# Performance work log

Measured on AMD Instinct MI355X. Metric: run time of the kernel, lower is better.

Reference implementation:

```python
import jax, jax.numpy as jnp
import numpy as np

# (a1,a2,a3,a4,b1,b2,b3,b4,xi_E,xi_I,mu,e,k) per oscillator type
PARAMS = {
    1: (0.0, 5.0, 5.0, 1.0, 0.0, -1.0, 1.0, 0.0, 0.0, 0.0, 5.0, 0.001, 500),
    2: (0.5, 0.55, 0.55, -0.5, 0.5, -0.55, -0.55, -0.5, 0.0, 0.0, 1.0, 0.001, 50),
    3: (0.5, 0.6, 0.55, 0.5, -0.5, -0.6, -0.55, 0.5, 0.0, 0.0, 1.0, 0.001, 50),
    4: (-0.5, 0.55, 0.55, -0.5, -0.5, -0.55, -0.55, 0.5, 0.0, 0.0, 1.0, 0.001, 50),
    5: (-0.9, 0.9, 0.9, -0.9, 0.9, -0.9, -0.9, 0.9, 0.0, 0.0, 1.0, 0.001, 50),
    6: (-0.9, 0.9, 0.9, -0.9, 0.9, -0.9, -0.9, 0.9, 0.0, 0.0, 1.0, 0.001, 300),
    7: (-5.0, 5.0, 5.0, -5.0, 1.0, -1.0, -1.0, 1.0, 0.0, 0.0, 1.0, 0.001, 50),
    8: (-5.0, 5.0, 5.0, -5.0, 1.0, -1.0, -1.0, 1.0, 0.0, 0.0, 1.0, 0.001, 300),
}
N_STEPS = 100  # torch runs t = 0..99 producing LORS[1..100], then max over those


def _lee_forward(x, osc_type):
    a1, a2, a3, a4, b1, b2, b3, b4, xi_E, xi_I, mu, e, k = PARAMS[osc_type]
    # stimulus with tiny sign-dependent offset; constant over time
    sim0 = x + e * jnp.sign(x)
    damp = jnp.exp(-k * sim0 * sim0)   # exp(-k*sim0^2), constant over time
    omega = jnp.tanh(mu * sim0)        # Omega[t+1] is the same every step
    E0 = jnp.full_like(x, 0.2)
    I0 = jnp.zeros_like(x)
    L0 = jnp.full_like(x, 0.2)
    m0 = jnp.full_like(x, -jnp.inf)    # running max over LORS[1..100]

    def step(carry, _):
        E, I, L, m = carry
        E1 = jnp.tanh(mu * (a1 * L + a2 * E - a3 * I + a4 * sim0 - xi_E))
        I1 = jnp.tanh(mu * (b1 * L - b2 * E - b3 * I + b4 * sim0 - xi_I))
        L1 = (E1 - I1) * damp + omega
        return (E1, I1, L1, jnp.maximum(m, L1)), None

    (_, _, _, m), _ = jax.lax.scan(step, (E0, I0, L0, m0), None, length=N_STEPS)
    return m


def setup_inputs() -> dict:
    key = jax.random.key(0)
    x = jax.random.normal(key, (2048, 512), dtype=jnp.float32)
    return {"x": x, "oscillator_type": 1}


def reference(x, oscillator_type):
    # output shape == x.shape: time-max-pooled LORS activation
    return _lee_forward(x, oscillator_type)
```

## Files before the change

### kernel.cpp

```cpp
#include <hip/hip_runtime.h>
#include <math.h>


#define N_STEPS 100

typedef float v2f __attribute__((ext_vector_type(2)));
__device__ __forceinline__ v2f splat2(float s){ v2f v; v.x = s; v.y = s; return v; }

__constant__ float PAR[8][13] = {
    { 0.0f,  5.0f,  5.0f,  1.0f,  0.0f, -1.0f,  1.0f,  0.0f, 0.0f, 0.0f, 5.0f, 0.001f, 500.0f},
    { 0.5f,  0.55f, 0.55f, -0.5f,  0.5f, -0.55f, -0.55f, -0.5f, 0.0f, 0.0f, 1.0f, 0.001f, 50.0f},
    { 0.5f,  0.6f,  0.55f,  0.5f, -0.5f, -0.6f,  -0.55f,  0.5f, 0.0f, 0.0f, 1.0f, 0.001f, 50.0f},
    {-0.5f,  0.55f, 0.55f, -0.5f, -0.5f, -0.55f, -0.55f,  0.5f, 0.0f, 0.0f, 1.0f, 0.001f, 50.0f},
    {-0.9f,  0.9f,  0.9f,  -0.9f,  0.9f, -0.9f,  -0.9f,   0.9f, 0.0f, 0.0f, 1.0f, 0.001f, 50.0f},
    {-0.9f,  0.9f,  0.9f,  -0.9f,  0.9f, -0.9f,  -0.9f,   0.9f, 0.0f, 0.0f, 1.0f, 0.001f, 300.0f},
    {-5.0f,  5.0f,  5.0f,  -5.0f,  1.0f, -1.0f,  -1.0f,   1.0f, 0.0f, 0.0f, 1.0f, 0.001f, 50.0f},
    {-5.0f,  5.0f,  5.0f,  -5.0f,  1.0f, -1.0f,  -1.0f,   1.0f, 0.0f, 0.0f, 1.0f, 0.001f, 300.0f},
};

__device__ __forceinline__ float xla_tanhf(float x) {
#pragma clang fp contract(off)
    float ax = fabsf(x);
    float xc = fminf(fmaxf(x, -7.99881172180175781f), 7.99881172180175781f);
    float x2 = xc * xc;
    float p = -2.76076847742355e-16f;
    p = fmaf(p, x2, 2.00018790482477e-13f);
    p = fmaf(p, x2, -8.60467152213735e-11f);
    p = fmaf(p, x2, 5.12229709037114e-08f);
    p = fmaf(p, x2, 1.48572235717979e-05f);
    p = fmaf(p, x2, 6.37261928875436e-04f);
    p = fmaf(p, x2, 4.89352455891786e-03f);
    float num = xc * p;
    float q = 1.19825839466702e-06f;
    q = fmaf(q, x2, 1.18534705686654e-04f);
    q = fmaf(q, x2, 2.26843463243900e-03f);
    q = fmaf(q, x2, 4.89352518554385e-03f);
    float r = num / q;
    return (ax < 0.0004f) ? x : r;
}

__device__ __forceinline__ v2f div2_exact(v2f a, v2f b) {
#pragma clang fp contract(off)
    v2f r;
    r.x = __builtin_amdgcn_rcpf(b.x);
    r.y = __builtin_amdgcn_rcpf(b.y);
    v2f one = splat2(1.0f);
    v2f nb; nb.x = -b.x; nb.y = -b.y;
    v2f e  = __builtin_elementwise_fma(nb, r, one);
    r = __builtin_elementwise_fma(e, r, r);
    v2f e2 = __builtin_elementwise_fma(nb, r, one);
    r = __builtin_elementwise_fma(e2, r, r);
    v2f y = a * r;
    v2f rem = __builtin_elementwise_fma(nb, y, a);
    y = __builtin_elementwise_fma(rem, r, y);
    return y;
}

__device__ __forceinline__ v2f xla_tanh2(v2f x) {
#pragma clang fp contract(off)
    const float C = 7.99881172180175781f;
    v2f xc = __builtin_elementwise_min(__builtin_elementwise_max(x, splat2(-C)), splat2(C));
    v2f x2 = xc * xc;
    v2f p = splat2(-2.76076847742355e-16f);
    p = __builtin_elementwise_fma(p, x2, splat2(2.00018790482477e-13f));
    p = __builtin_elementwise_fma(p, x2, splat2(-8.60467152213735e-11f));
    p = __builtin_elementwise_fma(p, x2, splat2(5.12229709037114e-08f));
    p = __builtin_elementwise_fma(p, x2, splat2(1.48572235717979e-05f));
    p = __builtin_elementwise_fma(p, x2, splat2(6.37261928875436e-04f));
    p = __builtin_elementwise_fma(p, x2, splat2(4.89352455891786e-03f));
    v2f num = xc * p;
    v2f q = splat2(1.19825839466702e-06f);
    q = __builtin_elementwise_fma(q, x2, splat2(1.18534705686654e-04f));
    q = __builtin_elementwise_fma(q, x2, splat2(2.26843463243900e-03f));
    q = __builtin_elementwise_fma(q, x2, splat2(4.89352518554385e-03f));
    v2f d = div2_exact(num, q);
    v2f r;
    r.x = (fabsf(x.x) < 0.0004f) ? x.x : d.x;
    r.y = (fabsf(x.y) < 0.0004f) ? x.y : d.y;
    return r;
}

__device__ __forceinline__ float xla_expf(float x) {
#pragma clang fp contract(off)
    float xc = fminf(fmaxf(x, -88.3762626647949f), 88.3762626647950f);
    float fx = floorf(fmaf(xc, 1.44269504088896341f, 0.5f));
    float r = fmaf(fx, -0.693359375f, xc);
    r = fmaf(fx, 2.12194440e-4f, r);
    float r2 = r * r;
    float y = 1.9875691500e-4f;
    y = fmaf(y, r, 1.3981999507e-3f);
    y = fmaf(y, r, 8.3334519073e-3f);
    y = fmaf(y, r, 4.1665795894e-2f);
    y = fmaf(y, r, 1.6666665459e-1f);
    y = fmaf(y, r, 5.0000001201e-1f);
    y = fmaf(y, r2, r);
    y = y + 1.0f;
    int n2 = (int)fx;
    float p2n = __int_as_float((n2 + 127) << 23);
    return y * p2n;
}

__device__ __forceinline__ void preamble(float xv, const float* p,
                                         float& sim0, float& damp, float& omega) {
#pragma clang fp contract(off)
    float mu = p[10], e = p[11], k = p[12];
    float sgn  = (xv > 0.0f) ? 1.0f : ((xv < 0.0f) ? -1.0f : 0.0f);
    sim0 = fmaf(e, sgn, xv);
    float targ = (-k * sim0) * sim0;
    damp  = xla_expf(targ);
    omega = xla_tanhf(mu * sim0);
}

__device__ __forceinline__ bool fast_omega(float damp, float omega) {
    return (2.0f * damp) < (fabsf(omega) * 0x1p-26f);
}

__device__ __forceinline__ bool slow_t1(float xv, float e) {
#pragma clang fp contract(off)
    float sgn  = (xv > 0.0f) ? 1.0f : ((xv < 0.0f) ? -1.0f : 0.0f);
    float sim0 = fmaf(e, sgn, xv);
    return fabsf(sim0) <= 0.21f;
}

__device__ __forceinline__ float loop_t1(float sim0, float damp, float omega) {
#pragma clang fp contract(off)
    float E = 0.2f, I = 0.0f;
    float Dmax = -INFINITY;
    for (int s = 0; s < N_STEPS; ++s) {
        float tE = 5.0f * E;
        v2f mulc; mulc.x = -5.0f; mulc.y = -1.0f;
        v2f iv   = splat2(I);
        v2f addv; addv.x = tE;    addv.y = E;
        v2f u = __builtin_elementwise_fma(mulc, iv, addv);
        float sE = u.x + sim0;
        v2f pre; pre.x = sE; pre.y = u.y;
        v2f args = splat2(5.0f) * pre;
        v2f t = xla_tanh2(args);
        float D = t.x - t.y;
        Dmax = fmaxf(Dmax, D);
        E = t.x; I = t.y;
    }
    return fmaf(Dmax, damp, omega);
}

__device__ __forceinline__ float loop_gen(const float* p, float sim0,
                                          float damp, float omega) {
#pragma clang fp contract(off)
    float a1 = p[0], a2 = p[1], a3 = p[2], a4 = p[3];
    float b1 = p[4], b2 = p[5], b3 = p[6], b4 = p[7];
    float xiE = p[8], xiI = p[9], mu = p[10];
    float nb2 = -b2;
    float E = 0.2f, I = 0.0f, L = 0.2f;
    float m = -INFINITY;
    for (int s = 0; s < N_STEPS; ++s) {
        float tE = a2 * E;
        float uE = fmaf(a1, L, tE);
        uE = fmaf(-a3, I, uE);
        uE = fmaf(a4, sim0, uE);
        uE = uE - xiE;
        float argE = mu * uE;
        float tI = nb2 * E;
        float uI = fmaf(b1, L, tI);
        uI = fmaf(-b3, I, uI);
        uI = fmaf(b4, sim0, uI);
        uI = uI - xiI;
        float argI = mu * uI;
        float E1 = xla_tanhf(argE);
        float I1 = xla_tanhf(argI);
        float d = E1 - I1;
        L = fmaf(d, damp, omega);
        E = E1; I = I1;
        m = fmaxf(m, L);
    }
    return m;
}

__device__ __forceinline__ bool classify_slow(float xv, int t, const float* p) {
    if (t == 1) return slow_t1(xv, p[11]);
    float sim0, damp, omega;
    preamble(xv, p, sim0, damp, omega);
    return !fast_omega(damp, omega);
}


__global__ __launch_bounds__(256)
void k_count(const float* __restrict__ x, const int* __restrict__ osc_type,
             unsigned* __restrict__ bcount, int n)
{
    __shared__ unsigned wc[4];
    int i = blockIdx.x * 256 + threadIdx.x;
    int t = *osc_type;
    const float* p = PAR[t - 1];
    bool slow = (i < n) && classify_slow(x[i], t, p);
    unsigned long long mask = __ballot(slow);
    int lane = threadIdx.x & 63, wid = threadIdx.x >> 6;
    if (lane == 0) wc[wid] = (unsigned)__popcll(mask);
    __syncthreads();
    if (threadIdx.x == 0) bcount[blockIdx.x] = wc[0] + wc[1] + wc[2] + wc[3];
}

__global__ __launch_bounds__(256)
void k_fill(const float* __restrict__ x, const int* __restrict__ osc_type,
            float* __restrict__ out, unsigned* __restrict__ bcount,
            unsigned* __restrict__ wl, int n, int NB)
{
#pragma clang fp contract(off)
    __shared__ unsigned sums[256];
    __shared__ unsigned woff[4];
    int tid = threadIdx.x;
    int bid = blockIdx.x;

    unsigned s = 0;
    for (int j = tid; j < bid; j += 256) s += bcount[j];
    sums[tid] = s;
    __syncthreads();
    for (int off = 128; off > 0; off >>= 1) {
        if (tid < off) sums[tid] += sums[tid + off];
        __syncthreads();
    }
    unsigned bbase = sums[0];

    int i = bid * 256 + tid;
    bool active = (i < n);
    int t = *osc_type;
    const float* p = PAR[t - 1];
    float xv = active ? x[i] : 1.0e9f;
    bool slow = active && classify_slow(xv, t, p);
    if (active && !slow) {
        float mu = p[10], e = p[11];
        float sgn  = (xv > 0.0f) ? 1.0f : ((xv < 0.0f) ? -1.0f : 0.0f);
        float sim0 = fmaf(e, sgn, xv);
        out[i] = xla_tanhf(mu * sim0);
    }
    unsigned long long mask = __ballot(slow);
    int lane = tid & 63, wid = tid >> 6;
    if (lane == 0) woff[wid] = (unsigned)__popcll(mask);
    __syncthreads();
    if (slow) {
        unsigned base = bbase;
        for (int w = 0; w < wid; ++w) base += woff[w];
        base += (unsigned)__popcll(mask & ((1ull << lane) - 1ull));
        wl[base] = (unsigned)i;
    }
    if (tid == 0 && bid == NB - 1)
        bcount[NB] = bbase + woff[0] + woff[1] + woff[2] + woff[3];
}

__global__ __launch_bounds__(64)
void k_process(const float* __restrict__ x, const int* __restrict__ osc_type,
               float* __restrict__ out, const unsigned* __restrict__ total_p,
               const unsigned* __restrict__ wl)
{
#pragma clang fp contract(off)
    unsigned total = *total_p;
    int t = *osc_type;
    const float* p = PAR[t - 1];
    unsigned stride = gridDim.x * 64u;
    for (unsigned tid = blockIdx.x * 64u + threadIdx.x; tid < total; tid += stride) {
        int i = (int)wl[tid];
        float sim0, damp, omega;
        preamble(x[i], p, sim0, damp, omega);
        out[i] = (t == 1) ? loop_t1(sim0, damp, omega)
                          : loop_gen(p, sim0, damp, omega);
    }
}

__global__ __launch_bounds__(256)
void k_monolithic(const float* __restrict__ x, const int* __restrict__ osc_type,
                  float* __restrict__ out, int n)
{
#pragma clang fp contract(off)
    int i = blockIdx.x * 256 + threadIdx.x;
    if (i >= n) return;
    int t = *osc_type;
    const float* p = PAR[t - 1];
    float sim0, damp, omega;
    preamble(x[i], p, sim0, damp, omega);
    if (fast_omega(damp, omega)) { out[i] = omega; return; }
    out[i] = (t == 1) ? loop_t1(sim0, damp, omega)
                      : loop_gen(p, sim0, damp, omega);
}

extern "C" void kernel_launch(void* const* d_in, const int* in_sizes, int n_in,
                              void* d_out, int out_size, void* d_ws, size_t ws_size,
                              hipStream_t stream) {
    const float* x        = (const float*)d_in[0];
    const int*   osc_type = (const int*)d_in[1];
    float*       out      = (float*)d_out;
    int n = in_sizes[0];
    int NB = (n + 255) / 256;

    size_t needed = ((size_t)NB + 1 + (size_t)n) * sizeof(unsigned);
    if (ws_size >= needed) {
        unsigned* bcount = (unsigned*)d_ws;
        unsigned* wl     = bcount + NB + 1;
        k_count  <<<NB, 256, 0, stream>>>(x, osc_type, bcount, n);
        k_fill   <<<NB, 256, 0, stream>>>(x, osc_type, out, bcount, wl, n, NB);
        k_process<<<4096, 64, 0, stream>>>(x, osc_type, out, bcount + NB, wl);
    } else {
        k_monolithic<<<NB, 256, 0, stream>>>(x, osc_type, out, n);
    }
}
```

Before: 42.03 us.

## Fuse count, fill and process into one kernel with block-local compaction

Replaces the three-kernel pipeline (count slow elements, global prefix-scan fill of a worklist, then a separate processing grid) with a single kernel. Each block classifies its 256 elements, writes fast results directly, and compacts slow elements' index, sim0, damp and omega into shared memory. One wavefront then runs the 100-step loops over that local list. This removes two launches, the per-block O(NB) prefix summation and the global worklist traffic. The cost is that load balancing is confined to each block, and three of the four waves sit idle during the loop.

```diff
diff --git a/kernel.cpp b/kernel.cpp
--- a/kernel.cpp
+++ b/kernel.cpp
@@ -115,10 +115,7 @@
     return (2.0f * damp) < (fabsf(omega) * 0x1p-26f);
 }
 
-__device__ __forceinline__ bool slow_t1(float xv, float e) {
-#pragma clang fp contract(off)
-    float sgn  = (xv > 0.0f) ? 1.0f : ((xv < 0.0f) ? -1.0f : 0.0f);
-    float sim0 = fmaf(e, sgn, xv);
+__device__ __forceinline__ bool slow_t1_from_sim0(float sim0) {
     return fabsf(sim0) <= 0.21f;
 }
 
@@ -175,110 +172,51 @@
     return m;
 }
 
-__device__ __forceinline__ bool classify_slow(float xv, int t, const float* p) {
-    if (t == 1) return slow_t1(xv, p[11]);
-    float sim0, damp, omega;
-    preamble(xv, p, sim0, damp, omega);
-    return !fast_omega(damp, omega);
-}
-
-
 __global__ __launch_bounds__(256)
-void k_count(const float* __restrict__ x, const int* __restrict__ osc_type,
-             unsigned* __restrict__ bcount, int n)
+void k_fused(const float* __restrict__ x, const int* __restrict__ osc_type,
+             float* __restrict__ out, int n)
 {
+#pragma clang fp contract(off)
     __shared__ unsigned wc[4];
-    int i = blockIdx.x * 256 + threadIdx.x;
-    int t = *osc_type;
-    const float* p = PAR[t - 1];
-    bool slow = (i < n) && classify_slow(x[i], t, p);
-    unsigned long long mask = __ballot(slow);
-    int lane = threadIdx.x & 63, wid = threadIdx.x >> 6;
-    if (lane == 0) wc[wid] = (unsigned)__popcll(mask);
-    __syncthreads();
-    if (threadIdx.x == 0) bcount[blockIdx.x] = wc[0] + wc[1] + wc[2] + wc[3];
-}
-
-__global__ __launch_bounds__(256)
-void k_fill(const float* __restrict__ x, const int* __restrict__ osc_type,
-            float* __restrict__ out, unsigned* __restrict__ bcount,
-            unsigned* __restrict__ wl, int n, int NB)
-{
-#pragma clang fp contract(off)
-    __shared__ unsigned sums[256];
-    __shared__ unsigned woff[4];
+    __shared__ unsigned sidx[256];
+    __shared__ float    ssim[256], sdamp[256], somega[256];
+
     int tid = threadIdx.x;
-    int bid = blockIdx.x;
-
-    unsigned s = 0;
-    for (int j = tid; j < bid; j += 256) s += bcount[j];
-    sums[tid] = s;
-    __syncthreads();
-    for (int off = 128; off > 0; off >>= 1) {
-        if (tid < off) sums[tid] += sums[tid + off];
-        __syncthreads();
-    }
-    unsigned bbase = sums[0];
-
-    int i = bid * 256 + tid;
+    int i = blockIdx.x * 256 + tid;
     bool active = (i < n);
     int t = *osc_type;
     const float* p = PAR[t - 1];
+
     float xv = active ? x[i] : 1.0e9f;
-    bool slow = active && classify_slow(xv, t, p);
-    if (active && !slow) {
-        float mu = p[10], e = p[11];
-        float sgn  = (xv > 0.0f) ? 1.0f : ((xv < 0.0f) ? -1.0f : 0.0f);
-        float sim0 = fmaf(e, sgn, xv);
-        out[i] = xla_tanhf(mu * sim0);
-    }
+    float sim0, damp, omega;
+    preamble(xv, p, sim0, damp, omega);
+    bool slow;
+    if (t == 1) slow = active && slow_t1_from_sim0(sim0);
+    else        slow = active && !fast_omega(damp, omega);
+    if (active && !slow) out[i] = omega;
+
     unsigned long long mask = __ballot(slow);
     int lane = tid & 63, wid = tid >> 6;
-    if (lane == 0) woff[wid] = (unsigned)__popcll(mask);
+    if (lane == 0) wc[wid] = (unsigned)__popcll(mask);
     __syncthreads();
     if (slow) {
-        unsigned base = bbase;
-        for (int w = 0; w < wid; ++w) base += woff[w];
-        base += (unsigned)__popcll(mask & ((1ull << lane) - 1ull));
-        wl[base] = (unsigned)i;
-    }
-    if (tid == 0 && bid == NB - 1)
-        bcount[NB] = bbase + woff[0] + woff[1] + woff[2] + woff[3];
-}
-
-__global__ __launch_bounds__(64)
-void k_process(const float* __restrict__ x, const int* __restrict__ osc_type,
-               float* __restrict__ out, const unsigned* __restrict__ total_p,
-               const unsigned* __restrict__ wl)
-{
-#pragma clang fp contract(off)
-    unsigned total = *total_p;
-    int t = *osc_type;
-    const float* p = PAR[t - 1];
-    unsigned stride = gridDim.x * 64u;
-    for (unsigned tid = blockIdx.x * 64u + threadIdx.x; tid < total; tid += stride) {
-        int i = (int)wl[tid];
-        float sim0, damp, omega;
-        preamble(x[i], p, sim0, damp, omega);
-        out[i] = (t == 1) ? loop_t1(sim0, damp, omega)
-                          : loop_gen(p, sim0, damp, omega);
-    }
-}
-
-__global__ __launch_bounds__(256)
-void k_monolithic(const float* __restrict__ x, const int* __restrict__ osc_type,
-                  float* __restrict__ out, int n)
-{
-#pragma clang fp contract(off)
-    int i = blockIdx.x * 256 + threadIdx.x;
-    if (i >= n) return;
-    int t = *osc_type;
-    const float* p = PAR[t - 1];
-    float sim0, damp, omega;
-    preamble(x[i], p, sim0, damp, omega);
-    if (fast_omega(damp, omega)) { out[i] = omega; return; }
-    out[i] = (t == 1) ? loop_t1(sim0, damp, omega)
-                      : loop_gen(p, sim0, damp, omega);
+        unsigned pos = 0;
+        for (int w = 0; w < wid; ++w) pos += wc[w];
+        pos += (unsigned)__popcll(mask & ((1ull << lane) - 1ull));
+        sidx[pos]  = (unsigned)i;
+        ssim[pos]  = sim0;
+        sdamp[pos] = damp;
+        somega[pos] = omega;
+    }
+    __syncthreads();
+    if (tid >= 64) return;
+
+    unsigned S = wc[0] + wc[1] + wc[2] + wc[3];
+    for (unsigned j = (unsigned)tid; j < S; j += 64u) {
+        float r = (t == 1) ? loop_t1(ssim[j], sdamp[j], somega[j])
+                           : loop_gen(p, ssim[j], sdamp[j], somega[j]);
+        out[sidx[j]] = r;
+    }
 }
 
 extern "C" void kernel_launch(void* const* d_in, const int* in_sizes, int n_in,
@@ -290,14 +228,5 @@
     int n = in_sizes[0];
     int NB = (n + 255) / 256;
 
-    size_t needed = ((size_t)NB + 1 + (size_t)n) * sizeof(unsigned);
-    if (ws_size >= needed) {
-        unsigned* bcount = (unsigned*)d_ws;
-        unsigned* wl     = bcount + NB + 1;
-        k_count  <<<NB, 256, 0, stream>>>(x, osc_type, bcount, n);
-        k_fill   <<<NB, 256, 0, stream>>>(x, osc_type, out, bcount, wl, n, NB);
-        k_process<<<4096, 64, 0, stream>>>(x, osc_type, out, bcount + NB, wl);
-    } else {
-        k_monolithic<<<NB, 256, 0, stream>>>(x, osc_type, out, n);
-    }
-}
+    k_fused<<<NB, 256, 0, stream>>>(x, osc_type, out, n);
+}
```

Result: faster. 40.99 us (-2.5%).
